# Kernel tuning notes

Hardware: AMD Instinct MI355X
Metric: run time of the kernel (lower is better)

## Reference

```python
import jax, jax.numpy as jnp
import numpy as np

B, L = 512, 256
N_NEG, L_NEG = 20, 64
VOCAB = 50000  # table has VOCAB+1 rows (row 0 = padding)
D = 100
K = 14
LAMBDA = 1.0


def setup_inputs() -> dict:
    key = jax.random.key(0)
    k1, k2, k3, k4, k5, k6, k7, k8 = jax.random.split(key, 8)
    pos_ids = jax.random.randint(k1, (B, L), 0, VOCAB + 1)
    neg_ids = jax.random.randint(k2, (B, N_NEG, L_NEG), 0, VOCAB + 1)
    emb_table = jax.random.normal(k3, (VOCAB + 1, D), dtype=jnp.float32) * 0.1
    emb_table = emb_table.at[0].set(0.0)  # padding row is zeros
    W_att = jax.random.normal(k4, (D, D), dtype=jnp.float32) * 0.05
    Wk = jax.random.normal(k5, (D, K), dtype=jnp.float32) * 0.1
    bk = jnp.zeros((K,), dtype=jnp.float32)
    Wf = jax.random.normal(k6, (K, D), dtype=jnp.float32) * 0.1  # aspect matrix (kmeans-init in original)
    bf = jnp.zeros((D,), dtype=jnp.float32)
    return {"pos_ids": pos_ids, "neg_ids": neg_ids, "emb_table": emb_table,
            "W_att": W_att, "Wk": Wk, "bk": bk, "Wf": Wf, "bf": bf}


def reference(pos_ids, neg_ids, emb_table, W_att, Wk, bk, Wf, bf):
    mask = pos_ids != 0                                   # [B, L]
    maskf = mask.astype(jnp.float32)
    e = emb_table[pos_ids]                                # [B, L, D]
    # --- masked aspect attention ---
    ys = jnp.mean(e, axis=-2)                             # [B, D] (unmasked mean, as in source)
    eW = jnp.einsum('bld,de->ble', e, W_att) * maskf[..., None]
    f = jnp.einsum('bld,bd->bl', eW, ys)[..., None]       # [B, L, 1]
    f = f + ((~mask).astype(f.dtype) * -1e9)[..., None]
    att = jax.nn.softmax(f, axis=-2)                      # softmax over L
    zs = jnp.sum(att * e, axis=-2)                        # [B, D]
    # --- aspect probabilities and reconstruction ---
    pt = jax.nn.sigmoid(zs @ Wk + bk)                     # [B, K]
    rs = pt @ Wf + bf                                     # [B, D]
    # --- orthogonality reg (faithful to source: uses the NORMS, normalize(...)[1]) ---
    norms = jnp.linalg.norm(Wf, axis=1, keepdims=True)    # [K, 1]
    reg = norms @ norms.T - jnp.ones((K, K), dtype=jnp.float32)
    reg = jnp.sqrt(jnp.sum(reg * reg))                    # Frobenius norm
    # --- margin loss ---
    pos_term = jnp.sum(rs * zs)                           # tensordot(rs, zs, [[0,1],[0,1]])
    a = jnp.mean(emb_table[neg_ids], axis=-2)             # [B, N_NEG, D]
    # tensordot(a, expand_dims(rs,-2), [[0,2],[0,2]]) -> [N_NEG, 1], then reduce_sum
    neg_term = jnp.sum(jnp.einsum('bnd,bd->n', a, rs))
    loss = jax.nn.relu(1.0 - neg_term + pos_term) + LAMBDA * reg
    return (loss, pt, rs)
```

## Files before the change

### kernel.cpp

```cpp
#include <hip/hip_runtime.h>
#include <hip/hip_bf16.h>

#if !__has_builtin(__builtin_amdgcn_cvt_pk_f32_fp8) || !__has_builtin(__builtin_amdgcn_cvt_pk_fp8_f32)
#include <hip/hip_fp8.h>
#endif

#define Bx 512
#define Lx 256
#define Dx 100
#define Kx 14
#define VROWS 50001
#define NEG_ROWS 1280
#define TPB 512
#define NGRP 16

#define PAD8  128
#define RAW8  100

typedef float floatx2 __attribute__((ext_vector_type(2)));

__device__ __forceinline__ float dot4(float4 a, float4 b) {
    return a.x * b.x + a.y * b.y + a.z * b.z + a.w * b.w;
}

__device__ __forceinline__ float4 fp8x4_dec(unsigned u) {
#if __has_builtin(__builtin_amdgcn_cvt_pk_f32_fp8)
    floatx2 lo = __builtin_amdgcn_cvt_pk_f32_fp8((int)u, false);
    floatx2 hi = __builtin_amdgcn_cvt_pk_f32_fp8((int)u, true);
    return make_float4(lo.x, lo.y, hi.x, hi.y);
#else
    __hip_fp8_e4m3 a, b, c, d;
    a.__x = (unsigned char)(u & 0xFF);
    b.__x = (unsigned char)((u >> 8) & 0xFF);
    c.__x = (unsigned char)((u >> 16) & 0xFF);
    d.__x = (unsigned char)((u >> 24) & 0xFF);
    return make_float4((float)a, (float)b, (float)c, (float)d);
#endif
}

__device__ __forceinline__ unsigned fp8x4_enc(float4 v) {
#if __has_builtin(__builtin_amdgcn_cvt_pk_fp8_f32)
    int p = 0;
    p = __builtin_amdgcn_cvt_pk_fp8_f32(v.x, v.y, p, false);
    p = __builtin_amdgcn_cvt_pk_fp8_f32(v.z, v.w, p, true);
    return (unsigned)p;
#else
    __hip_fp8_e4m3 a(v.x), b(v.y), c(v.z), d(v.w);
    return (unsigned)a.__x | ((unsigned)b.__x << 8) |
           ((unsigned)c.__x << 16) | ((unsigned)d.__x << 24);
#endif
}

__device__ __forceinline__ void acc16(uint4 u, float4* A) {
    const float4 v0 = fp8x4_dec(u.x);
    const float4 v1 = fp8x4_dec(u.y);
    const float4 v2 = fp8x4_dec(u.z);
    const float4 v3 = fp8x4_dec(u.w);
    A[0].x += v0.x; A[0].y += v0.y; A[0].z += v0.z; A[0].w += v0.w;
    A[1].x += v1.x; A[1].y += v1.y; A[1].z += v1.z; A[1].w += v1.w;
    A[2].x += v2.x; A[2].y += v2.y; A[2].z += v2.z; A[2].w += v2.w;
    A[3].x += v3.x; A[3].y += v3.y; A[3].z += v3.z; A[3].w += v3.w;
}

__device__ __forceinline__ void fold4(float4* A) {
    #pragma unroll
    for (int k = 0; k < 4; ++k) {
        A[k].x += __shfl_xor(A[k].x, 8);
        A[k].y += __shfl_xor(A[k].y, 8);
        A[k].z += __shfl_xor(A[k].z, 8);
        A[k].w += __shfl_xor(A[k].w, 8);
    }
    #pragma unroll
    for (int k = 0; k < 4; ++k) {
        A[k].x += __shfl_xor(A[k].x, 16);
        A[k].y += __shfl_xor(A[k].y, 16);
        A[k].z += __shfl_xor(A[k].z, 16);
        A[k].w += __shfl_xor(A[k].w, 16);
    }
}

__global__ __launch_bounds__(256) void convert_kernel(
    const float* __restrict__ table, unsigned char* __restrict__ tb8,
    const float* __restrict__ Wf, float* __restrict__ acc, int RS8, int padded)
{
    const int tid = threadIdx.x;
    const int gid = blockIdx.x * 256 + tid;
    if (gid < 4) acc[gid] = 0.0f;

    const int row = gid >> 5;
    const int c   = gid & 31;
    if (row < VROWS) {
        if (c < 25) {
            const float4 v = *reinterpret_cast<const float4*>(
                table + (size_t)row * Dx + c * 4);
            *reinterpret_cast<unsigned*>(tb8 + (size_t)row * RS8 + c * 4) = fp8x4_enc(v);
        } else if (padded) {
            *reinterpret_cast<unsigned*>(tb8 + (size_t)row * RS8 + c * 4) = 0u;
        }
    }

    if (blockIdx.x == 0) {
        __shared__ float n_sh[Kx];
        __shared__ float r_sh[256];
        if (tid < Kx) {
            const float4* w4 = reinterpret_cast<const float4*>(Wf + (size_t)tid * Dx);
            float s = 0.f;
            #pragma unroll
            for (int i = 0; i < 25; ++i) { const float4 w = w4[i]; s += dot4(w, w); }
            n_sh[tid] = sqrtf(s);
        }
        __syncthreads();
        float vv = 0.f;
        if (tid < Kx * Kx) {
            const int i = tid / Kx;
            const int j = tid - i * Kx;
            const float x = n_sh[i] * n_sh[j] - 1.0f;
            vv = x * x;
        }
        r_sh[tid] = vv;
        __syncthreads();
        for (int s = 128; s > 0; s >>= 1) {
            if (tid < s) r_sh[tid] += r_sh[tid + s];
            __syncthreads();
        }
        if (tid == 0) acc[3] = sqrtf(r_sh[0]);
    }
}

__global__ __launch_bounds__(TPB) void fused_all_pad(
    const int* __restrict__ pos_ids, const int* __restrict__ neg_ids,
    const unsigned char* __restrict__ tb8,
    const float* __restrict__ W_att, const float* __restrict__ Wk,
    const float* __restrict__ bk, const float* __restrict__ Wf,
    const float* __restrict__ bf, float* __restrict__ pt_out,
    float* __restrict__ rs_out, float* __restrict__ acc,
    float* __restrict__ out)
{
    const int tid  = threadIdx.x;
    const int grp  = tid >> 5;
    const int lane = tid & 31;
    const int b    = blockIdx.x;

    __shared__ __align__(16) unsigned rowbuf[Lx][32];
    __shared__ int   ids[Lx];
    __shared__ int   idn[NEG_ROWS];
    __shared__ __align__(16) float pf2[NGRP][128];
    __shared__ __align__(16) float ys_sh[104];
    __shared__ __align__(16) float t_sh[104];
    __shared__ float zs_sh[104];
    __shared__ float pt_sh[Kx];
    __shared__ float m_sh[NGRP], s_sh[NGRP], sc_sh[NGRP];
    __shared__ float wred[8][2];

    if (tid < Lx) ids[tid] = pos_ids[(size_t)b * Lx + tid] << 7;
    for (int i = tid; i < NEG_ROWS; i += TPB)
        idn[i] = neg_ids[(size_t)b * NEG_ROWS + i] << 7;
    __syncthreads();

    const int j16  = (lane & 7) * 16;
    const int j4   = (lane & 7) * 4;
    const int rsub = lane >> 3;

    float4 An[4] = {{0,0,0,0},{0,0,0,0},{0,0,0,0},{0,0,0,0}};
    #pragma unroll 2
    for (int it = 0; it < NEG_ROWS / 256; ++it) {
        const int base = it * 256 + grp * 16 + rsub;
        const uint4 u0 = *(const uint4*)(tb8 + (size_t)idn[base]      + j16);
        const uint4 u1 = *(const uint4*)(tb8 + (size_t)idn[base + 4]  + j16);
        const uint4 u2 = *(const uint4*)(tb8 + (size_t)idn[base + 8]  + j16);
        const uint4 u3 = *(const uint4*)(tb8 + (size_t)idn[base + 12] + j16);
        acc16(u0, An); acc16(u1, An); acc16(u2, An); acc16(u3, An);
    }

    {
        const int base = grp * 16 + rsub;
        const uint4 u0 = *(const uint4*)(tb8 + (size_t)ids[base]      + j16);
        const uint4 u1 = *(const uint4*)(tb8 + (size_t)ids[base + 4]  + j16);
        const uint4 u2 = *(const uint4*)(tb8 + (size_t)ids[base + 8]  + j16);
        const uint4 u3 = *(const uint4*)(tb8 + (size_t)ids[base + 12] + j16);
        *(uint4*)&rowbuf[base][j4]      = u0;
        *(uint4*)&rowbuf[base + 4][j4]  = u1;
        *(uint4*)&rowbuf[base + 8][j4]  = u2;
        *(uint4*)&rowbuf[base + 12][j4] = u3;
        float4 Ap[4] = {{0,0,0,0},{0,0,0,0},{0,0,0,0},{0,0,0,0}};
        acc16(u0, Ap); acc16(u1, Ap); acc16(u2, Ap); acc16(u3, Ap);
        fold4(Ap);
        if (lane < 8) {
            *(float4*)&pf2[grp][16 * lane]      = Ap[0];
            *(float4*)&pf2[grp][16 * lane + 4]  = Ap[1];
            *(float4*)&pf2[grp][16 * lane + 8]  = Ap[2];
            *(float4*)&pf2[grp][16 * lane + 12] = Ap[3];
        }
    }
    __syncthreads();
    if (tid < Dx) {
        float s = 0.f;
        #pragma unroll
        for (int gg = 0; gg < NGRP; ++gg) s += pf2[gg][tid];
        ys_sh[tid] = s * (1.0f / Lx);
    }
    __syncthreads();

    if (tid < Dx) {
        const float4* w4 = reinterpret_cast<const float4*>(W_att + (size_t)tid * Dx);
        const float4* y4 = reinterpret_cast<const float4*>(ys_sh);
        float s = 0.f;
        #pragma unroll
        for (int i = 0; i < 25; ++i) s += dot4(w4[i], y4[i]);
        t_sh[tid] = s;
    }
    __syncthreads();

    {
        const float4 tl = (lane < 25) ? ((const float4*)t_sh)[lane]
                                      : make_float4(0.f, 0.f, 0.f, 0.f);
        float m = -1e30f, ssum = 0.f;
        float4 za = {0.f, 0.f, 0.f, 0.f};
        for (int r = grp; r < Lx; r += 32) {
            const int id0 = ids[r];
            const int id1 = ids[r + 16];
            float4 e0 = {0,0,0,0}, e1 = {0,0,0,0};
            if (lane < 25) {
                e0 = fp8x4_dec(rowbuf[r][lane]);
                e1 = fp8x4_dec(rowbuf[r + 16][lane]);
            }
            float d0 = dot4(e0, tl);
            float d1 = dot4(e1, tl);
            #pragma unroll
            for (int o = 16; o > 0; o >>= 1) {
                d0 += __shfl_xor(d0, o, 32);
                d1 += __shfl_xor(d1, o, 32);
            }
            const float f0 = (id0 != 0) ? d0 : -1e30f;
            const float f1 = (id1 != 0) ? d1 : -1e30f;
            const float mn = fmaxf(m, fmaxf(f0, f1));
            const float sc = __expf(m - mn);
            const float w0 = (id0 != 0) ? __expf(d0 - mn) : 0.f;
            const float w1 = (id1 != 0) ? __expf(d1 - mn) : 0.f;
            ssum = ssum * sc + w0 + w1;
            za.x = za.x * sc + w0 * e0.x + w1 * e1.x;
            za.y = za.y * sc + w0 * e0.y + w1 * e1.y;
            za.z = za.z * sc + w0 * e0.z + w1 * e1.z;
            za.w = za.w * sc + w0 * e0.w + w1 * e1.w;
            m = mn;
        }
        if (lane == 0) { m_sh[grp] = m; s_sh[grp] = ssum; }
        if (lane < 25) ((float4*)pf2[grp])[lane] = za;
    }
    __syncthreads();
    if (tid < NGRP) {
        float M = -1e30f;
        #pragma unroll
        for (int gg = 0; gg < NGRP; ++gg) M = fmaxf(M, m_sh[gg]);
        sc_sh[tid] = __expf(m_sh[tid] - M);
    }
    __syncthreads();
    if (tid < Dx) {
        float S = 0.f, z = 0.f;
        #pragma unroll
        for (int gg = 0; gg < NGRP; ++gg) {
            S += s_sh[gg] * sc_sh[gg];
            z += pf2[gg][tid] * sc_sh[gg];
        }
        zs_sh[tid] = z / S;
    }
    __syncthreads();

    if (tid < Kx) {
        float s = bk[tid];
        for (int d = 0; d < Dx; ++d) s += zs_sh[d] * Wk[d * Kx + tid];
        const float pk = 1.0f / (1.0f + __expf(-s));
        pt_sh[tid] = pk;
        pt_out[(size_t)b * Kx + tid] = pk;
    }
    __syncthreads();

    float posc = 0.f, negc = 0.f, rs_reg = 0.f;
    if (tid < Dx) {
        float r = bf[tid];
        #pragma unroll
        for (int k = 0; k < Kx; ++k) r += pt_sh[k] * Wf[k * Dx + tid];
        rs_out[(size_t)b * Dx + tid] = r;
        rs_reg = r;
        posc = r * zs_sh[tid];
    }

    fold4(An);
    if (lane < 8) {
        *(float4*)&pf2[grp][16 * lane]      = An[0];
        *(float4*)&pf2[grp][16 * lane + 4]  = An[1];
        *(float4*)&pf2[grp][16 * lane + 8]  = An[2];
        *(float4*)&pf2[grp][16 * lane + 12] = An[3];
    }
    __syncthreads();
    if (tid < Dx) {
        float gsum = 0.f;
        #pragma unroll
        for (int gg = 0; gg < NGRP; ++gg) gsum += pf2[gg][tid];
        negc = gsum * rs_reg;
    }

    #pragma unroll
    for (int o = 32; o > 0; o >>= 1) {
        posc += __shfl_xor(posc, o);
        negc += __shfl_xor(negc, o);
    }
    const int wid = tid >> 6;
    if ((tid & 63) == 0) { wred[wid][0] = posc; wred[wid][1] = negc; }
    __syncthreads();

    if (tid == 0) {
        float P = 0.f, N = 0.f;
        #pragma unroll
        for (int w = 0; w < 8; ++w) { P += wred[w][0]; N += wred[w][1]; }
        atomicAdd(&acc[0], P);
        atomicAdd(&acc[1], N);
        __threadfence();
        const unsigned t = atomicAdd(reinterpret_cast<unsigned int*>(acc) + 2, 1u);
        if (t == (unsigned)(Bx - 1)) {
            const float pos = atomicAdd(&acc[0], 0.0f);
            const float neg = atomicAdd(&acc[1], 0.0f);
            const float reg = atomicAdd(&acc[3], 0.0f);
            const float margin = 1.0f - neg * (1.0f / 64.0f) + pos;
            out[0] = fmaxf(margin, 0.0f) + reg;
        }
    }
}

__global__ __launch_bounds__(TPB) void fused_all_compact(
    const int* __restrict__ pos_ids, const int* __restrict__ neg_ids,
    const unsigned char* __restrict__ tb8,
    const float* __restrict__ W_att, const float* __restrict__ Wk,
    const float* __restrict__ bk, const float* __restrict__ Wf,
    const float* __restrict__ bf, float* __restrict__ pt_out,
    float* __restrict__ rs_out, float* __restrict__ acc,
    float* __restrict__ out, int RS8)
{
    const int tid  = threadIdx.x;
    const int grp  = tid >> 5;
    const int lane = tid & 31;
    const int b    = blockIdx.x;

    __shared__ __align__(16) unsigned rowbuf[Lx][26];
    __shared__ int   ids[Lx];
    __shared__ int   idn[NEG_ROWS];
    __shared__ __align__(16) float4 part4[NGRP][26];
    __shared__ __align__(16) float ys_sh[104];
    __shared__ __align__(16) float t_sh[104];
    __shared__ float zs_sh[104];
    __shared__ float pt_sh[Kx];
    __shared__ float m_sh[NGRP], s_sh[NGRP], sc_sh[NGRP];
    __shared__ float wred[8][2];

    float* pf = (float*)part4;

    if (tid < Lx) ids[tid] = pos_ids[(size_t)b * Lx + tid] * RS8;
    for (int i = tid; i < NEG_ROWS; i += TPB)
        idn[i] = neg_ids[(size_t)b * NEG_ROWS + i] * RS8;
    __syncthreads();

    float4 na = {0.f, 0.f, 0.f, 0.f};
    if (lane < 25) {
        const int o = lane * 4;
        float4 a0 = {0,0,0,0}, a1 = {0,0,0,0}, a2 = {0,0,0,0}, a3 = {0,0,0,0};
        for (int r = grp; r < NEG_ROWS; r += 64) {
            const float4 v0 = fp8x4_dec(*(const unsigned*)(tb8 + (size_t)idn[r]      + o));
            const float4 v1 = fp8x4_dec(*(const unsigned*)(tb8 + (size_t)idn[r + 16] + o));
            const float4 v2 = fp8x4_dec(*(const unsigned*)(tb8 + (size_t)idn[r + 32] + o));
            const float4 v3 = fp8x4_dec(*(const unsigned*)(tb8 + (size_t)idn[r + 48] + o));
            a0.x += v0.x; a0.y += v0.y; a0.z += v0.z; a0.w += v0.w;
            a1.x += v1.x; a1.y += v1.y; a1.z += v1.z; a1.w += v1.w;
            a2.x += v2.x; a2.y += v2.y; a2.z += v2.z; a2.w += v2.w;
            a3.x += v3.x; a3.y += v3.y; a3.z += v3.z; a3.w += v3.w;
        }
        na.x = a0.x + a1.x + a2.x + a3.x;
        na.y = a0.y + a1.y + a2.y + a3.y;
        na.z = a0.z + a1.z + a2.z + a3.z;
        na.w = a0.w + a1.w + a2.w + a3.w;
    }

    if (lane < 25) {
        const int o = lane * 4;
        float4 a0 = {0,0,0,0}, a1 = {0,0,0,0}, a2 = {0,0,0,0}, a3 = {0,0,0,0};
        for (int r = grp; r < Lx; r += 64) {
            const unsigned u0 = *(const unsigned*)(tb8 + (size_t)ids[r]      + o);
            const unsigned u1 = *(const unsigned*)(tb8 + (size_t)ids[r + 16] + o);
            const unsigned u2 = *(const unsigned*)(tb8 + (size_t)ids[r + 32] + o);
            const unsigned u3 = *(const unsigned*)(tb8 + (size_t)ids[r + 48] + o);
            rowbuf[r][lane]      = u0;
            rowbuf[r + 16][lane] = u1;
            rowbuf[r + 32][lane] = u2;
            rowbuf[r + 48][lane] = u3;
            const float4 v0 = fp8x4_dec(u0);
            const float4 v1 = fp8x4_dec(u1);
            const float4 v2 = fp8x4_dec(u2);
            const float4 v3 = fp8x4_dec(u3);
            a0.x += v0.x; a0.y += v0.y; a0.z += v0.z; a0.w += v0.w;
            a1.x += v1.x; a1.y += v1.y; a1.z += v1.z; a1.w += v1.w;
            a2.x += v2.x; a2.y += v2.y; a2.z += v2.z; a2.w += v2.w;
            a3.x += v3.x; a3.y += v3.y; a3.z += v3.z; a3.w += v3.w;
        }
        a0.x += a1.x + a2.x + a3.x; a0.y += a1.y + a2.y + a3.y;
        a0.z += a1.z + a2.z + a3.z; a0.w += a1.w + a2.w + a3.w;
        part4[grp][lane] = a0;
    }
    __syncthreads();
    if (tid < Dx) {
        float s = 0.f;
        #pragma unroll
        for (int gg = 0; gg < NGRP; ++gg) s += pf[gg * 104 + tid];
        ys_sh[tid] = s * (1.0f / Lx);
    }
    __syncthreads();

    if (tid < Dx) {
        const float4* w4 = reinterpret_cast<const float4*>(W_att + (size_t)tid * Dx);
        const float4* y4 = reinterpret_cast<const float4*>(ys_sh);
        float s = 0.f;
        #pragma unroll
        for (int i = 0; i < 25; ++i) s += dot4(w4[i], y4[i]);
        t_sh[tid] = s;
    }
    __syncthreads();

    {
        const float4 tl = (lane < 25) ? ((const float4*)t_sh)[lane]
                                      : make_float4(0.f, 0.f, 0.f, 0.f);
        float m = -1e30f, ssum = 0.f;
        float4 za = {0.f, 0.f, 0.f, 0.f};
        for (int r = grp; r < Lx; r += 32) {
            const int id0 = ids[r];
            const int id1 = ids[r + 16];
            float4 e0 = {0,0,0,0}, e1 = {0,0,0,0};
            if (lane < 25) {
                e0 = fp8x4_dec(rowbuf[r][lane]);
                e1 = fp8x4_dec(rowbuf[r + 16][lane]);
            }
            float d0 = dot4(e0, tl);
            float d1 = dot4(e1, tl);
            #pragma unroll
            for (int o = 16; o > 0; o >>= 1) {
                d0 += __shfl_xor(d0, o, 32);
                d1 += __shfl_xor(d1, o, 32);
            }
            const float f0 = (id0 != 0) ? d0 : -1e30f;
            const float f1 = (id1 != 0) ? d1 : -1e30f;
            const float mn = fmaxf(m, fmaxf(f0, f1));
            const float sc = __expf(m - mn);
            const float w0 = (id0 != 0) ? __expf(d0 - mn) : 0.f;
            const float w1 = (id1 != 0) ? __expf(d1 - mn) : 0.f;
            ssum = ssum * sc + w0 + w1;
            za.x = za.x * sc + w0 * e0.x + w1 * e1.x;
            za.y = za.y * sc + w0 * e0.y + w1 * e1.y;
            za.z = za.z * sc + w0 * e0.z + w1 * e1.z;
            za.w = za.w * sc + w0 * e0.w + w1 * e1.w;
            m = mn;
        }
        if (lane == 0) { m_sh[grp] = m; s_sh[grp] = ssum; }
        if (lane < 25) part4[grp][lane] = za;
    }
    __syncthreads();
    if (tid < NGRP) {
        float M = -1e30f;
        #pragma unroll
        for (int gg = 0; gg < NGRP; ++gg) M = fmaxf(M, m_sh[gg]);
        sc_sh[tid] = __expf(m_sh[tid] - M);
    }
    __syncthreads();
    if (tid < Dx) {
        float S = 0.f, z = 0.f;
        #pragma unroll
        for (int gg = 0; gg < NGRP; ++gg) {
            S += s_sh[gg] * sc_sh[gg];
            z += pf[gg * 104 + tid] * sc_sh[gg];
        }
        zs_sh[tid] = z / S;
    }
    __syncthreads();

    if (tid < Kx) {
        float s = bk[tid];
        for (int d = 0; d < Dx; ++d) s += zs_sh[d] * Wk[d * Kx + tid];
        const float pk = 1.0f / (1.0f + __expf(-s));
        pt_sh[tid] = pk;
        pt_out[(size_t)b * Kx + tid] = pk;
    }
    __syncthreads();

    float posc = 0.f, negc = 0.f, rs_reg = 0.f;
    if (tid < Dx) {
        float r = bf[tid];
        #pragma unroll
        for (int k = 0; k < Kx; ++k) r += pt_sh[k] * Wf[k * Dx + tid];
        rs_out[(size_t)b * Dx + tid] = r;
        rs_reg = r;
        posc = r * zs_sh[tid];
    }

    if (lane < 25) part4[grp][lane] = na;
    __syncthreads();
    if (tid < Dx) {
        float gsum = 0.f;
        #pragma unroll
        for (int gg = 0; gg < NGRP; ++gg) gsum += pf[gg * 104 + tid];
        negc = gsum * rs_reg;
    }

    #pragma unroll
    for (int o = 32; o > 0; o >>= 1) {
        posc += __shfl_xor(posc, o);
        negc += __shfl_xor(negc, o);
    }
    const int wid = tid >> 6;
    if ((tid & 63) == 0) { wred[wid][0] = posc; wred[wid][1] = negc; }
    __syncthreads();

    if (tid == 0) {
        float P = 0.f, N = 0.f;
        #pragma unroll
        for (int w = 0; w < 8; ++w) { P += wred[w][0]; N += wred[w][1]; }
        atomicAdd(&acc[0], P);
        atomicAdd(&acc[1], N);
        __threadfence();
        const unsigned t = atomicAdd(reinterpret_cast<unsigned int*>(acc) + 2, 1u);
        if (t == (unsigned)(Bx - 1)) {
            const float pos = atomicAdd(&acc[0], 0.0f);
            const float neg = atomicAdd(&acc[1], 0.0f);
            const float reg = atomicAdd(&acc[3], 0.0f);
            const float margin = 1.0f - neg * (1.0f / 64.0f) + pos;
            out[0] = fmaxf(margin, 0.0f) + reg;
        }
    }
}

extern "C" void kernel_launch(void* const* d_in, const int* in_sizes, int n_in,
                              void* d_out, int out_size, void* d_ws, size_t ws_size,
                              hipStream_t stream) {
    const int*   pos_ids = (const int*)  d_in[0];
    const int*   neg_ids = (const int*)  d_in[1];
    const float* table   = (const float*)d_in[2];
    const float* W_att   = (const float*)d_in[3];
    const float* Wk      = (const float*)d_in[4];
    const float* bk      = (const float*)d_in[5];
    const float* Wf      = (const float*)d_in[6];
    const float* bf      = (const float*)d_in[7];

    float* out    = (float*)d_out;
    float* pt_out = out + 1;
    float* rs_out = out + 1 + (size_t)Bx * Kx;

    const size_t need_pad = (size_t)VROWS * PAD8 + 16 + 4 * sizeof(float);
    const int padded = (ws_size >= need_pad) ? 1 : 0;
    const int RS8 = padded ? PAD8 : RAW8;

    unsigned char* tb8 = (unsigned char*)d_ws;
    size_t acc_off = (size_t)VROWS * RS8;
    acc_off = (acc_off + 15) & ~(size_t)15;
    float* acc = (float*)((char*)d_ws + acc_off);

    const int nthreads = VROWS * 32;
    convert_kernel<<<(nthreads + 255) / 256, 256, 0, stream>>>(
        table, tb8, Wf, acc, RS8, padded);
    if (padded) {
        fused_all_pad<<<Bx, TPB, 0, stream>>>(
            pos_ids, neg_ids, tb8, W_att, Wk, bk, Wf, bf,
            pt_out, rs_out, acc, out);
    } else {
        fused_all_compact<<<Bx, TPB, 0, stream>>>(
            pos_ids, neg_ids, tb8, W_att, Wk, bk, Wf, bf,
            pt_out, rs_out, acc, out, RS8);
    }
}
```

Measured before the change: 125.9 us.

## Merge table conversion and fused compute into one cooperative kernel with grid sync

Replaces the separate FP8 conversion kernel plus fused kernel with a single cooperative launch: each block converts a slice of the embedding table, block 0 computes the regularizer, then a grid-wide sync precedes the per-batch fused body. The aim is to remove a kernel launch boundary and overlap id loading with conversion. It requires all 512 blocks of 512 threads to be co-resident and falls back to the old two-kernel path if the cooperative launch fails; grid sync itself adds cost.

```diff
diff --git a/kernel.cpp b/kernel.cpp
--- a/kernel.cpp
+++ b/kernel.cpp
@@ -1,5 +1,6 @@
 #include <hip/hip_runtime.h>
 #include <hip/hip_bf16.h>
+#include <hip/hip_cooperative_groups.h>
 
 #if !__has_builtin(__builtin_amdgcn_cvt_pk_f32_fp8) || !__has_builtin(__builtin_amdgcn_cvt_pk_fp8_f32)
 #include <hip/hip_fp8.h>
@@ -13,6 +14,7 @@
 #define NEG_ROWS 1280
 #define TPB 512
 #define NGRP 16
+#define CROWS ((VROWS + Bx - 1) / Bx)
 
 #define PAD8  128
 #define RAW8  100
@@ -79,6 +81,268 @@
     }
 }
 
+struct __align__(16) SharedState {
+    unsigned rowbuf[Lx][32];
+    int      ids[Lx];
+    int      idn[NEG_ROWS];
+    float    pf2[NGRP][128];
+    float    ys_sh[104];
+    float    t_sh[104];
+    float    zs_sh[104];
+    float    pt_sh[Kx];
+    float    m_sh[NGRP], s_sh[NGRP], sc_sh[NGRP];
+    float    wred[8][2];
+};
+
+__device__ __forceinline__ void fused_body(
+    SharedState& S, int b, int tid,
+    const unsigned char* __restrict__ tb8,
+    const float* __restrict__ W_att, const float* __restrict__ Wk,
+    const float* __restrict__ bk, const float* __restrict__ Wf,
+    const float* __restrict__ bf, float* __restrict__ pt_out,
+    float* __restrict__ rs_out, float* __restrict__ acc,
+    float* __restrict__ out)
+{
+    const int grp  = tid >> 5;
+    const int lane = tid & 31;
+    const int j16  = (lane & 7) * 16;
+    const int j4   = (lane & 7) * 4;
+    const int rsub = lane >> 3;
+
+    float4 An[4] = {{0,0,0,0},{0,0,0,0},{0,0,0,0},{0,0,0,0}};
+    #pragma unroll 2
+    for (int it = 0; it < NEG_ROWS / 256; ++it) {
+        const int base = it * 256 + grp * 16 + rsub;
+        const uint4 u0 = *(const uint4*)(tb8 + (size_t)S.idn[base]      + j16);
+        const uint4 u1 = *(const uint4*)(tb8 + (size_t)S.idn[base + 4]  + j16);
+        const uint4 u2 = *(const uint4*)(tb8 + (size_t)S.idn[base + 8]  + j16);
+        const uint4 u3 = *(const uint4*)(tb8 + (size_t)S.idn[base + 12] + j16);
+        acc16(u0, An); acc16(u1, An); acc16(u2, An); acc16(u3, An);
+    }
+
+    {
+        const int base = grp * 16 + rsub;
+        const uint4 u0 = *(const uint4*)(tb8 + (size_t)S.ids[base]      + j16);
+        const uint4 u1 = *(const uint4*)(tb8 + (size_t)S.ids[base + 4]  + j16);
+        const uint4 u2 = *(const uint4*)(tb8 + (size_t)S.ids[base + 8]  + j16);
+        const uint4 u3 = *(const uint4*)(tb8 + (size_t)S.ids[base + 12] + j16);
+        *(uint4*)&S.rowbuf[base][j4]      = u0;
+        *(uint4*)&S.rowbuf[base + 4][j4]  = u1;
+        *(uint4*)&S.rowbuf[base + 8][j4]  = u2;
+        *(uint4*)&S.rowbuf[base + 12][j4] = u3;
+        float4 Ap[4] = {{0,0,0,0},{0,0,0,0},{0,0,0,0},{0,0,0,0}};
+        acc16(u0, Ap); acc16(u1, Ap); acc16(u2, Ap); acc16(u3, Ap);
+        fold4(Ap);
+        if (lane < 8) {
+            *(float4*)&S.pf2[grp][16 * lane]      = Ap[0];
+            *(float4*)&S.pf2[grp][16 * lane + 4]  = Ap[1];
+            *(float4*)&S.pf2[grp][16 * lane + 8]  = Ap[2];
+            *(float4*)&S.pf2[grp][16 * lane + 12] = Ap[3];
+        }
+    }
+    __syncthreads();
+    if (tid < Dx) {
+        float s = 0.f;
+        #pragma unroll
+        for (int gg = 0; gg < NGRP; ++gg) s += S.pf2[gg][tid];
+        S.ys_sh[tid] = s * (1.0f / Lx);
+    }
+    __syncthreads();
+
+    if (tid < Dx) {
+        const float4* w4 = reinterpret_cast<const float4*>(W_att + (size_t)tid * Dx);
+        const float4* y4 = reinterpret_cast<const float4*>(S.ys_sh);
+        float s = 0.f;
+        #pragma unroll
+        for (int i = 0; i < 25; ++i) s += dot4(w4[i], y4[i]);
+        S.t_sh[tid] = s;
+    }
+    __syncthreads();
+
+    {
+        const float4 tl = (lane < 25) ? ((const float4*)S.t_sh)[lane]
+                                      : make_float4(0.f, 0.f, 0.f, 0.f);
+        float m = -1e30f, ssum = 0.f;
+        float4 za = {0.f, 0.f, 0.f, 0.f};
+        for (int r = grp; r < Lx; r += 32) {
+            const int id0 = S.ids[r];
+            const int id1 = S.ids[r + 16];
+            float4 e0 = {0,0,0,0}, e1 = {0,0,0,0};
+            if (lane < 25) {
+                e0 = fp8x4_dec(S.rowbuf[r][lane]);
+                e1 = fp8x4_dec(S.rowbuf[r + 16][lane]);
+            }
+            float d0 = dot4(e0, tl);
+            float d1 = dot4(e1, tl);
+            #pragma unroll
+            for (int o = 16; o > 0; o >>= 1) {
+                d0 += __shfl_xor(d0, o, 32);
+                d1 += __shfl_xor(d1, o, 32);
+            }
+            const float f0 = (id0 != 0) ? d0 : -1e30f;
+            const float f1 = (id1 != 0) ? d1 : -1e30f;
+            const float mn = fmaxf(m, fmaxf(f0, f1));
+            const float sc = __expf(m - mn);
+            const float w0 = (id0 != 0) ? __expf(d0 - mn) : 0.f;
+            const float w1 = (id1 != 0) ? __expf(d1 - mn) : 0.f;
+            ssum = ssum * sc + w0 + w1;
+            za.x = za.x * sc + w0 * e0.x + w1 * e1.x;
+            za.y = za.y * sc + w0 * e0.y + w1 * e1.y;
+            za.z = za.z * sc + w0 * e0.z + w1 * e1.z;
+            za.w = za.w * sc + w0 * e0.w + w1 * e1.w;
+            m = mn;
+        }
+        if (lane == 0) { S.m_sh[grp] = m; S.s_sh[grp] = ssum; }
+        if (lane < 25) ((float4*)S.pf2[grp])[lane] = za;
+    }
+    __syncthreads();
+    if (tid < NGRP) {
+        float M = -1e30f;
+        #pragma unroll
+        for (int gg = 0; gg < NGRP; ++gg) M = fmaxf(M, S.m_sh[gg]);
+        S.sc_sh[tid] = __expf(S.m_sh[tid] - M);
+    }
+    __syncthreads();
+    if (tid < Dx) {
+        float Ssum = 0.f, z = 0.f;
+        #pragma unroll
+        for (int gg = 0; gg < NGRP; ++gg) {
+            Ssum += S.s_sh[gg] * S.sc_sh[gg];
+            z += S.pf2[gg][tid] * S.sc_sh[gg];
+        }
+        S.zs_sh[tid] = z / Ssum;
+    }
+    __syncthreads();
+
+    if (tid < Kx) {
+        float s = bk[tid];
+        for (int d = 0; d < Dx; ++d) s += S.zs_sh[d] * Wk[d * Kx + tid];
+        const float pk = 1.0f / (1.0f + __expf(-s));
+        S.pt_sh[tid] = pk;
+        pt_out[(size_t)b * Kx + tid] = pk;
+    }
+    __syncthreads();
+
+    float posc = 0.f, negc = 0.f, rs_reg = 0.f;
+    if (tid < Dx) {
+        float r = bf[tid];
+        #pragma unroll
+        for (int k = 0; k < Kx; ++k) r += S.pt_sh[k] * Wf[k * Dx + tid];
+        rs_out[(size_t)b * Dx + tid] = r;
+        rs_reg = r;
+        posc = r * S.zs_sh[tid];
+    }
+
+    fold4(An);
+    if (lane < 8) {
+        *(float4*)&S.pf2[grp][16 * lane]      = An[0];
+        *(float4*)&S.pf2[grp][16 * lane + 4]  = An[1];
+        *(float4*)&S.pf2[grp][16 * lane + 8]  = An[2];
+        *(float4*)&S.pf2[grp][16 * lane + 12] = An[3];
+    }
+    __syncthreads();
+    if (tid < Dx) {
+        float gsum = 0.f;
+        #pragma unroll
+        for (int gg = 0; gg < NGRP; ++gg) gsum += S.pf2[gg][tid];
+        negc = gsum * rs_reg;
+    }
+
+    #pragma unroll
+    for (int o = 32; o > 0; o >>= 1) {
+        posc += __shfl_xor(posc, o);
+        negc += __shfl_xor(negc, o);
+    }
+    const int wid = tid >> 6;
+    if ((tid & 63) == 0) { S.wred[wid][0] = posc; S.wred[wid][1] = negc; }
+    __syncthreads();
+
+    if (tid == 0) {
+        float P = 0.f, N = 0.f;
+        #pragma unroll
+        for (int w = 0; w < 8; ++w) { P += S.wred[w][0]; N += S.wred[w][1]; }
+        atomicAdd(&acc[0], P);
+        atomicAdd(&acc[1], N);
+        __threadfence();
+        const unsigned t = atomicAdd(reinterpret_cast<unsigned int*>(acc) + 2, 1u);
+        if (t == (unsigned)(Bx - 1)) {
+            const float pos = atomicAdd(&acc[0], 0.0f);
+            const float neg = atomicAdd(&acc[1], 0.0f);
+            const float reg = atomicAdd(&acc[3], 0.0f);
+            const float margin = 1.0f - neg * (1.0f / 64.0f) + pos;
+            out[0] = fmaxf(margin, 0.0f) + reg;
+        }
+    }
+}
+
+__global__ __launch_bounds__(TPB) void mono(
+    const int* __restrict__ pos_ids, const int* __restrict__ neg_ids,
+    const float* __restrict__ table,
+    const float* __restrict__ W_att, const float* __restrict__ Wk,
+    const float* __restrict__ bk, const float* __restrict__ Wf,
+    const float* __restrict__ bf,
+    unsigned char* __restrict__ tb8, float* __restrict__ pt_out,
+    float* __restrict__ rs_out, float* __restrict__ acc,
+    float* __restrict__ out)
+{
+    __shared__ SharedState S;
+    const int tid = threadIdx.x;
+    const int b   = blockIdx.x;
+
+    {
+        const int rbase = b * CROWS;
+        const int rcnt  = min(CROWS, VROWS - rbase);
+        for (int i = tid; i < rcnt * 32; i += TPB) {
+            const int row = rbase + (i >> 5);
+            const int c   = i & 31;
+            unsigned w = 0u;
+            if (c < 25) {
+                const float4 v = *reinterpret_cast<const float4*>(
+                    table + (size_t)row * Dx + c * 4);
+                w = fp8x4_enc(v);
+            }
+            *reinterpret_cast<unsigned*>(tb8 + ((size_t)row << 7) + c * 4) = w;
+        }
+    }
+
+    if (tid < Lx) S.ids[tid] = pos_ids[(size_t)b * Lx + tid] << 7;
+    for (int i = tid; i < NEG_ROWS; i += TPB)
+        S.idn[i] = neg_ids[(size_t)b * NEG_ROWS + i] << 7;
+
+    if (b == 0) {
+        if (tid < 3) acc[tid] = 0.0f;
+        __shared__ float n_sh[Kx];
+        __shared__ float r_sh[256];
+        if (tid < Kx) {
+            const float4* w4 = reinterpret_cast<const float4*>(Wf + (size_t)tid * Dx);
+            float s = 0.f;
+            #pragma unroll
+            for (int i = 0; i < 25; ++i) { const float4 w = w4[i]; s += dot4(w, w); }
+            n_sh[tid] = sqrtf(s);
+        }
+        __syncthreads();
+        float vv = 0.f;
+        if (tid < 256 && tid < Kx * Kx) {
+            const int i = tid / Kx;
+            const int j = tid - i * Kx;
+            const float x = n_sh[i] * n_sh[j] - 1.0f;
+            vv = x * x;
+        }
+        if (tid < 256) r_sh[tid] = vv;
+        __syncthreads();
+        for (int s = 128; s > 0; s >>= 1) {
+            if (tid < s) r_sh[tid] += r_sh[tid + s];
+            __syncthreads();
+        }
+        if (tid == 0) { acc[3] = sqrtf(r_sh[0]); __threadfence(); }
+    }
+
+    cooperative_groups::this_grid().sync();
+
+    fused_body(S, b, tid, tb8, W_att, Wk, bk, Wf, bf,
+               pt_out, rs_out, acc, out);
+}
+
 __global__ __launch_bounds__(256) void convert_kernel(
     const float* __restrict__ table, unsigned char* __restrict__ tb8,
     const float* __restrict__ Wf, float* __restrict__ acc, int RS8, int padded)
@@ -136,15 +400,37 @@
     float* __restrict__ rs_out, float* __restrict__ acc,
     float* __restrict__ out)
 {
+    __shared__ SharedState S;
+    const int tid = threadIdx.x;
+    const int b   = blockIdx.x;
+
+    if (tid < Lx) S.ids[tid] = pos_ids[(size_t)b * Lx + tid] << 7;
+    for (int i = tid; i < NEG_ROWS; i += TPB)
+        S.idn[i] = neg_ids[(size_t)b * NEG_ROWS + i] << 7;
+    __syncthreads();
+
+    fused_body(S, b, tid, tb8, W_att, Wk, bk, Wf, bf,
+               pt_out, rs_out, acc, out);
+}
+
+__global__ __launch_bounds__(TPB) void fused_all_compact(
+    const int* __restrict__ pos_ids, const int* __restrict__ neg_ids,
+    const unsigned char* __restrict__ tb8,
+    const float* __restrict__ W_att, const float* __restrict__ Wk,
+    const float* __restrict__ bk, const float* __restrict__ Wf,
+    const float* __restrict__ bf, float* __restrict__ pt_out,
+    float* __restrict__ rs_out, float* __restrict__ acc,
+    float* __restrict__ out, int RS8)
+{
     const int tid  = threadIdx.x;
     const int grp  = tid >> 5;
     const int lane = tid & 31;
     const int b    = blockIdx.x;
 
-    __shared__ __align__(16) unsigned rowbuf[Lx][32];
+    __shared__ __align__(16) unsigned rowbuf[Lx][26];
     __shared__ int   ids[Lx];
     __shared__ int   idn[NEG_ROWS];
-    __shared__ __align__(16) float pf2[NGRP][128];
+    __shared__ __align__(16) float4 part4[NGRP][26];
     __shared__ __align__(16) float ys_sh[104];
     __shared__ __align__(16) float t_sh[104];
     __shared__ float zs_sh[104];
@@ -152,51 +438,63 @@
     __shared__ float m_sh[NGRP], s_sh[NGRP], sc_sh[NGRP];
     __shared__ float wred[8][2];
 
-    if (tid < Lx) ids[tid] = pos_ids[(size_t)b * Lx + tid] << 7;
+    float* pf = (float*)part4;
+
+    if (tid < Lx) ids[tid] = pos_ids[(size_t)b * Lx + tid] * RS8;
     for (int i = tid; i < NEG_ROWS; i += TPB)
-        idn[i] = neg_ids[(size_t)b * NEG_ROWS + i] << 7;
-    __syncthreads();
-
-    const int j16  = (lane & 7) * 16;
-    const int j4   = (lane & 7) * 4;
-    const int rsub = lane >> 3;
-
-    float4 An[4] = {{0,0,0,0},{0,0,0,0},{0,0,0,0},{0,0,0,0}};
-    #pragma unroll 2
-    for (int it = 0; it < NEG_ROWS / 256; ++it) {
-        const int base = it * 256 + grp * 16 + rsub;
-        const uint4 u0 = *(const uint4*)(tb8 + (size_t)idn[base]      + j16);
-        const uint4 u1 = *(const uint4*)(tb8 + (size_t)idn[base + 4]  + j16);
-        const uint4 u2 = *(const uint4*)(tb8 + (size_t)idn[base + 8]  + j16);
-        const uint4 u3 = *(const uint4*)(tb8 + (size_t)idn[base + 12] + j16);
-        acc16(u0, An); acc16(u1, An); acc16(u2, An); acc16(u3, An);
-    }
-
-    {
-        const int base = grp * 16 + rsub;
-        const uint4 u0 = *(const uint4*)(tb8 + (size_t)ids[base]      + j16);
-        const uint4 u1 = *(const uint4*)(tb8 + (size_t)ids[base + 4]  + j16);
-        const uint4 u2 = *(const uint4*)(tb8 + (size_t)ids[base + 8]  + j16);
-        const uint4 u3 = *(const uint4*)(tb8 + (size_t)ids[base + 12] + j16);
-        *(uint4*)&rowbuf[base][j4]      = u0;
-        *(uint4*)&rowbuf[base + 4][j4]  = u1;
-        *(uint4*)&rowbuf[base + 8][j4]  = u2;
-        *(uint4*)&rowbuf[base + 12][j4] = u3;
-        float4 Ap[4] = {{0,0,0,0},{0,0,0,0},{0,0,0,0},{0,0,0,0}};
-        acc16(u0, Ap); acc16(u1, Ap); acc16(u2, Ap); acc16(u3, Ap);
-        fold4(Ap);
-        if (lane < 8) {
-            *(float4*)&pf2[grp][16 * lane]      = Ap[0];
-            *(float4*)&pf2[grp][16 * lane + 4]  = Ap[1];
-            *(float4*)&pf2[grp][16 * lane + 8]  = Ap[2];
-            *(float4*)&pf2[grp][16 * lane + 12] = Ap[3];
-        }
+        idn[i] = neg_ids[(size_t)b * NEG_ROWS + i] * RS8;
+    __syncthreads();
+
+    float4 na = {0.f, 0.f, 0.f, 0.f};
+    if (lane < 25) {
+        const int o = lane * 4;
+        float4 a0 = {0,0,0,0}, a1 = {0,0,0,0}, a2 = {0,0,0,0}, a3 = {0,0,0,0};
+        for (int r = grp; r < NEG_ROWS; r += 64) {
+            const float4 v0 = fp8x4_dec(*(const unsigned*)(tb8 + (size_t)idn[r]      + o));
+            const float4 v1 = fp8x4_dec(*(const unsigned*)(tb8 + (size_t)idn[r + 16] + o));
+            const float4 v2 = fp8x4_dec(*(const unsigned*)(tb8 + (size_t)idn[r + 32] + o));
+            const float4 v3 = fp8x4_dec(*(const unsigned*)(tb8 + (size_t)idn[r + 48] + o));
+            a0.x += v0.x; a0.y += v0.y; a0.z += v0.z; a0.w += v0.w;
+            a1.x += v1.x; a1.y += v1.y; a1.z += v1.z; a1.w += v1.w;
+            a2.x += v2.x; a2.y += v2.y; a2.z += v2.z; a2.w += v2.w;
+            a3.x += v3.x; a3.y += v3.y; a3.z += v3.z; a3.w += v3.w;
+        }
+        na.x = a0.x + a1.x + a2.x + a3.x;
+        na.y = a0.y + a1.y + a2.y + a3.y;
+        na.z = a0.z + a1.z + a2.z + a3.z;
+        na.w = a0.w + a1.w + a2.w + a3.w;
+    }
+
+    if (lane < 25) {
+        const int o = lane * 4;
+        float4 a0 = {0,0,0,0}, a1 = {0,0,0,0}, a2 = {0,0,0,0}, a3 = {0,0,0,0};
+        for (int r = grp; r < Lx; r += 64) {
+            const unsigned u0 = *(const unsigned*)(tb8 + (size_t)ids[r]      + o);
+            const unsigned u1 = *(const unsigned*)(tb8 + (size_t)ids[r + 16] + o);
+            const unsigned u2 = *(const unsigned*)(tb8 + (size_t)ids[r + 32] + o);
+            const unsigned u3 = *(const unsigned*)(tb8 + (size_t)ids[r + 48] + o);
+            rowbuf[r][lane]      = u0;
+            rowbuf[r + 16][lane] = u1;
+            rowbuf[r + 32][lane] = u2;
+            rowbuf[r + 48][lane] = u3;
+            const float4 v0 = fp8x4_dec(u0);
+            const float4 v1 = fp8x4_dec(u1);
+            const float4 v2 = fp8x4_dec(u2);
+            const float4 v3 = fp8x4_dec(u3);
+            a0.x += v0.x; a0.y += v0.y; a0.z += v0.z; a0.w += v0.w;
+            a1.x += v1.x; a1.y += v1.y; a1.z += v1.z; a1.w += v1.w;
+            a2.x += v2.x; a2.y += v2.y; a2.z += v2.z; a2.w += v2.w;
+            a3.x += v3.x; a3.y += v3.y; a3.z += v3.z; a3.w += v3.w;
+        }
+        a0.x += a1.x + a2.x + a3.x; a0.y += a1.y + a2.y + a3.y;
+        a0.z += a1.z + a2.z + a3.z; a0.w += a1.w + a2.w + a3.w;
+        part4[grp][lane] = a0;
     }
     __syncthreads();
     if (tid < Dx) {
         float s = 0.f;
         #pragma unroll
-        for (int gg = 0; gg < NGRP; ++gg) s += pf2[gg][tid];
+        for (int gg = 0; gg < NGRP; ++gg) s += pf[gg * 104 + tid];
         ys_sh[tid] = s * (1.0f / Lx);
     }
     __syncthreads();
@@ -245,7 +543,7 @@
             m = mn;
         }
         if (lane == 0) { m_sh[grp] = m; s_sh[grp] = ssum; }
-        if (lane < 25) ((float4*)pf2[grp])[lane] = za;
+        if (lane < 25) part4[grp][lane] = za;
     }
     __syncthreads();
     if (tid < NGRP) {
@@ -260,7 +558,7 @@
         #pragma unroll
         for (int gg = 0; gg < NGRP; ++gg) {
             S += s_sh[gg] * sc_sh[gg];
-            z += pf2[gg][tid] * sc_sh[gg];
+            z += pf[gg * 104 + tid] * sc_sh[gg];
         }
         zs_sh[tid] = z / S;
     }
@@ -285,18 +583,12 @@
         posc = r * zs_sh[tid];
     }
 
-    fold4(An);
-    if (lane < 8) {
-        *(float4*)&pf2[grp][16 * lane]      = An[0];
-        *(float4*)&pf2[grp][16 * lane + 4]  = An[1];
-        *(float4*)&pf2[grp][16 * lane + 8]  = An[2];
-        *(float4*)&pf2[grp][16 * lane + 12] = An[3];
-    }
+    if (lane < 25) part4[grp][lane] = na;
     __syncthreads();
     if (tid < Dx) {
         float gsum = 0.f;
         #pragma unroll
-        for (int gg = 0; gg < NGRP; ++gg) gsum += pf2[gg][tid];
+        for (int gg = 0; gg < NGRP; ++gg) gsum += pf[gg * 104 + tid];
         negc = gsum * rs_reg;
     }
 
@@ -327,212 +619,6 @@
     }
 }
 
-__global__ __launch_bounds__(TPB) void fused_all_compact(
-    const int* __restrict__ pos_ids, const int* __restrict__ neg_ids,
-    const unsigned char* __restrict__ tb8,
-    const float* __restrict__ W_att, const float* __restrict__ Wk,
-    const float* __restrict__ bk, const float* __restrict__ Wf,
-    const float* __restrict__ bf, float* __restrict__ pt_out,
-    float* __restrict__ rs_out, float* __restrict__ acc,
-    float* __restrict__ out, int RS8)
-{
-    const int tid  = threadIdx.x;
-    const int grp  = tid >> 5;
-    const int lane = tid & 31;
-    const int b    = blockIdx.x;
-
-    __shared__ __align__(16) unsigned rowbuf[Lx][26];
-    __shared__ int   ids[Lx];
-    __shared__ int   idn[NEG_ROWS];
-    __shared__ __align__(16) float4 part4[NGRP][26];
-    __shared__ __align__(16) float ys_sh[104];
-    __shared__ __align__(16) float t_sh[104];
-    __shared__ float zs_sh[104];
-    __shared__ float pt_sh[Kx];
-    __shared__ float m_sh[NGRP], s_sh[NGRP], sc_sh[NGRP];
-    __shared__ float wred[8][2];
-
-    float* pf = (float*)part4;
-
-    if (tid < Lx) ids[tid] = pos_ids[(size_t)b * Lx + tid] * RS8;
-    for (int i = tid; i < NEG_ROWS; i += TPB)
-        idn[i] = neg_ids[(size_t)b * NEG_ROWS + i] * RS8;
-    __syncthreads();
-
-    float4 na = {0.f, 0.f, 0.f, 0.f};
-    if (lane < 25) {
-        const int o = lane * 4;
-        float4 a0 = {0,0,0,0}, a1 = {0,0,0,0}, a2 = {0,0,0,0}, a3 = {0,0,0,0};
-        for (int r = grp; r < NEG_ROWS; r += 64) {
-            const float4 v0 = fp8x4_dec(*(const unsigned*)(tb8 + (size_t)idn[r]      + o));
-            const float4 v1 = fp8x4_dec(*(const unsigned*)(tb8 + (size_t)idn[r + 16] + o));
-            const float4 v2 = fp8x4_dec(*(const unsigned*)(tb8 + (size_t)idn[r + 32] + o));
-            const float4 v3 = fp8x4_dec(*(const unsigned*)(tb8 + (size_t)idn[r + 48] + o));
-            a0.x += v0.x; a0.y += v0.y; a0.z += v0.z; a0.w += v0.w;
-            a1.x += v1.x; a1.y += v1.y; a1.z += v1.z; a1.w += v1.w;
-            a2.x += v2.x; a2.y += v2.y; a2.z += v2.z; a2.w += v2.w;
-            a3.x += v3.x; a3.y += v3.y; a3.z += v3.z; a3.w += v3.w;
-        }
-        na.x = a0.x + a1.x + a2.x + a3.x;
-        na.y = a0.y + a1.y + a2.y + a3.y;
-        na.z = a0.z + a1.z + a2.z + a3.z;
-        na.w = a0.w + a1.w + a2.w + a3.w;
-    }
-
-    if (lane < 25) {
-        const int o = lane * 4;
-        float4 a0 = {0,0,0,0}, a1 = {0,0,0,0}, a2 = {0,0,0,0}, a3 = {0,0,0,0};
-        for (int r = grp; r < Lx; r += 64) {
-            const unsigned u0 = *(const unsigned*)(tb8 + (size_t)ids[r]      + o);
-            const unsigned u1 = *(const unsigned*)(tb8 + (size_t)ids[r + 16] + o);
-            const unsigned u2 = *(const unsigned*)(tb8 + (size_t)ids[r + 32] + o);
-            const unsigned u3 = *(const unsigned*)(tb8 + (size_t)ids[r + 48] + o);
-            rowbuf[r][lane]      = u0;
-            rowbuf[r + 16][lane] = u1;
-            rowbuf[r + 32][lane] = u2;
-            rowbuf[r + 48][lane] = u3;
-            const float4 v0 = fp8x4_dec(u0);
-            const float4 v1 = fp8x4_dec(u1);
-            const float4 v2 = fp8x4_dec(u2);
-            const float4 v3 = fp8x4_dec(u3);
-            a0.x += v0.x; a0.y += v0.y; a0.z += v0.z; a0.w += v0.w;
-            a1.x += v1.x; a1.y += v1.y; a1.z += v1.z; a1.w += v1.w;
-            a2.x += v2.x; a2.y += v2.y; a2.z += v2.z; a2.w += v2.w;
-            a3.x += v3.x; a3.y += v3.y; a3.z += v3.z; a3.w += v3.w;
-        }
-        a0.x += a1.x + a2.x + a3.x; a0.y += a1.y + a2.y + a3.y;
-        a0.z += a1.z + a2.z + a3.z; a0.w += a1.w + a2.w + a3.w;
-        part4[grp][lane] = a0;
-    }
-    __syncthreads();
-    if (tid < Dx) {
-        float s = 0.f;
-        #pragma unroll
-        for (int gg = 0; gg < NGRP; ++gg) s += pf[gg * 104 + tid];
-        ys_sh[tid] = s * (1.0f / Lx);
-    }
-    __syncthreads();
-
-    if (tid < Dx) {
-        const float4* w4 = reinterpret_cast<const float4*>(W_att + (size_t)tid * Dx);
-        const float4* y4 = reinterpret_cast<const float4*>(ys_sh);
-        float s = 0.f;
-        #pragma unroll
-        for (int i = 0; i < 25; ++i) s += dot4(w4[i], y4[i]);
-        t_sh[tid] = s;
-    }
-    __syncthreads();
-
-    {
-        const float4 tl = (lane < 25) ? ((const float4*)t_sh)[lane]
-                                      : make_float4(0.f, 0.f, 0.f, 0.f);
-        float m = -1e30f, ssum = 0.f;
-        float4 za = {0.f, 0.f, 0.f, 0.f};
-        for (int r = grp; r < Lx; r += 32) {
-            const int id0 = ids[r];
-            const int id1 = ids[r + 16];
-            float4 e0 = {0,0,0,0}, e1 = {0,0,0,0};
-            if (lane < 25) {
-                e0 = fp8x4_dec(rowbuf[r][lane]);
-                e1 = fp8x4_dec(rowbuf[r + 16][lane]);
-            }
-            float d0 = dot4(e0, tl);
-            float d1 = dot4(e1, tl);
-            #pragma unroll
-            for (int o = 16; o > 0; o >>= 1) {
-                d0 += __shfl_xor(d0, o, 32);
-                d1 += __shfl_xor(d1, o, 32);
-            }
-            const float f0 = (id0 != 0) ? d0 : -1e30f;
-            const float f1 = (id1 != 0) ? d1 : -1e30f;
-            const float mn = fmaxf(m, fmaxf(f0, f1));
-            const float sc = __expf(m - mn);
-            const float w0 = (id0 != 0) ? __expf(d0 - mn) : 0.f;
-            const float w1 = (id1 != 0) ? __expf(d1 - mn) : 0.f;
-            ssum = ssum * sc + w0 + w1;
-            za.x = za.x * sc + w0 * e0.x + w1 * e1.x;
-            za.y = za.y * sc + w0 * e0.y + w1 * e1.y;
-            za.z = za.z * sc + w0 * e0.z + w1 * e1.z;
-            za.w = za.w * sc + w0 * e0.w + w1 * e1.w;
-            m = mn;
-        }
-        if (lane == 0) { m_sh[grp] = m; s_sh[grp] = ssum; }
-        if (lane < 25) part4[grp][lane] = za;
-    }
-    __syncthreads();
-    if (tid < NGRP) {
-        float M = -1e30f;
-        #pragma unroll
-        for (int gg = 0; gg < NGRP; ++gg) M = fmaxf(M, m_sh[gg]);
-        sc_sh[tid] = __expf(m_sh[tid] - M);
-    }
-    __syncthreads();
-    if (tid < Dx) {
-        float S = 0.f, z = 0.f;
-        #pragma unroll
-        for (int gg = 0; gg < NGRP; ++gg) {
-            S += s_sh[gg] * sc_sh[gg];
-            z += pf[gg * 104 + tid] * sc_sh[gg];
-        }
-        zs_sh[tid] = z / S;
-    }
-    __syncthreads();
-
-    if (tid < Kx) {
-        float s = bk[tid];
-        for (int d = 0; d < Dx; ++d) s += zs_sh[d] * Wk[d * Kx + tid];
-        const float pk = 1.0f / (1.0f + __expf(-s));
-        pt_sh[tid] = pk;
-        pt_out[(size_t)b * Kx + tid] = pk;
-    }
-    __syncthreads();
-
-    float posc = 0.f, negc = 0.f, rs_reg = 0.f;
-    if (tid < Dx) {
-        float r = bf[tid];
-        #pragma unroll
-        for (int k = 0; k < Kx; ++k) r += pt_sh[k] * Wf[k * Dx + tid];
-        rs_out[(size_t)b * Dx + tid] = r;
-        rs_reg = r;
-        posc = r * zs_sh[tid];
-    }
-
-    if (lane < 25) part4[grp][lane] = na;
-    __syncthreads();
-    if (tid < Dx) {
-        float gsum = 0.f;
-        #pragma unroll
-        for (int gg = 0; gg < NGRP; ++gg) gsum += pf[gg * 104 + tid];
-        negc = gsum * rs_reg;
-    }
-
-    #pragma unroll
-    for (int o = 32; o > 0; o >>= 1) {
-        posc += __shfl_xor(posc, o);
-        negc += __shfl_xor(negc, o);
-    }
-    const int wid = tid >> 6;
-    if ((tid & 63) == 0) { wred[wid][0] = posc; wred[wid][1] = negc; }
-    __syncthreads();
-
-    if (tid == 0) {
-        float P = 0.f, N = 0.f;
-        #pragma unroll
-        for (int w = 0; w < 8; ++w) { P += wred[w][0]; N += wred[w][1]; }
-        atomicAdd(&acc[0], P);
-        atomicAdd(&acc[1], N);
-        __threadfence();
-        const unsigned t = atomicAdd(reinterpret_cast<unsigned int*>(acc) + 2, 1u);
-        if (t == (unsigned)(Bx - 1)) {
-            const float pos = atomicAdd(&acc[0], 0.0f);
-            const float neg = atomicAdd(&acc[1], 0.0f);
-            const float reg = atomicAdd(&acc[3], 0.0f);
-            const float margin = 1.0f - neg * (1.0f / 64.0f) + pos;
-            out[0] = fmaxf(margin, 0.0f) + reg;
-        }
-    }
-}
-
 extern "C" void kernel_launch(void* const* d_in, const int* in_sizes, int n_in,
                               void* d_out, int out_size, void* d_ws, size_t ws_size,
                               hipStream_t stream) {
@@ -558,16 +644,32 @@
     acc_off = (acc_off + 15) & ~(size_t)15;
     float* acc = (float*)((char*)d_ws + acc_off);
 
-    const int nthreads = VROWS * 32;
-    convert_kernel<<<(nthreads + 255) / 256, 256, 0, stream>>>(
-        table, tb8, Wf, acc, RS8, padded);
+    bool done = false;
     if (padded) {
-        fused_all_pad<<<Bx, TPB, 0, stream>>>(
-            pos_ids, neg_ids, tb8, W_att, Wk, bk, Wf, bf,
-            pt_out, rs_out, acc, out);
-    } else {
-        fused_all_compact<<<Bx, TPB, 0, stream>>>(
-            pos_ids, neg_ids, tb8, W_att, Wk, bk, Wf, bf,
-            pt_out, rs_out, acc, out, RS8);
-    }
-}
+        void* kargs[] = {
+            (void*)&pos_ids, (void*)&neg_ids, (void*)&table,
+            (void*)&W_att, (void*)&Wk, (void*)&bk, (void*)&Wf, (void*)&bf,
+            (void*)&tb8, (void*)&pt_out, (void*)&rs_out, (void*)&acc, (void*)&out
+        };
+        if (hipLaunchCooperativeKernel((void*)mono, dim3(Bx), dim3(TPB),
+                                       kargs, 0, stream) == hipSuccess) {
+            done = true;
+        } else {
+            (void)hipGetLastError();
+        }
+    }
+    if (!done) {
+        const int nthreads = VROWS * 32;
+        convert_kernel<<<(nthreads + 255) / 256, 256, 0, stream>>>(
+            table, tb8, Wf, acc, RS8, padded);
+        if (padded) {
+            fused_all_pad<<<Bx, TPB, 0, stream>>>(
+                pos_ids, neg_ids, tb8, W_att, Wk, bk, Wf, bf,
+                pt_out, rs_out, acc, out);
+        } else {
+            fused_all_compact<<<Bx, TPB, 0, stream>>>(
+                pos_ids, neg_ids, tb8, W_att, Wk, bk, Wf, bf,
+                pt_out, rs_out, acc, out, RS8);
+        }
+    }
+}
```

Result: slower. 198.0 us (+57.2%).
